# Performance work log

Measured on AMD Instinct MI355X. Metric: run time of the kernel, lower is better.

Reference implementation:

```python
import jax, jax.numpy as jnp
import numpy as np

N = 50000      # nodes
E = 800000     # edges
IN, HID, OUT = 256, 512, 256
EPS = 1e-5     # BatchNorm eps


def setup_inputs() -> dict:
    key = jax.random.key(0)
    ks = jax.random.split(key, 12)
    x = jax.random.normal(ks[0], (N, IN), jnp.float32)
    edge_index = jax.random.randint(ks[1], (2, E), 0, N, jnp.int32)

    def lin(k, fi, fo):
        return jax.random.normal(k, (fi, fo), jnp.float32) / np.sqrt(fi).astype(np.float32)

    return {
        "x": x,
        "edge_index": edge_index,
        "W1": lin(ks[2], IN, HID),  "b1": jnp.zeros((HID,), jnp.float32),
        "g1": jnp.ones((HID,), jnp.float32), "be1": jnp.zeros((HID,), jnp.float32),
        "W2": lin(ks[3], HID, HID), "b2": jnp.zeros((HID,), jnp.float32),
        "g2": jnp.ones((HID,), jnp.float32), "be2": jnp.zeros((HID,), jnp.float32),
        "W3": lin(ks[4], HID, OUT), "b3": jnp.zeros((OUT,), jnp.float32),
    }


def _gcn_conv(x, W, b, src, dst, dinv):
    # PyG GCNConv: D^{-1/2}(A+I)D^{-1/2} X W + b, edge weights = 1
    h = x @ W                                   # [N, F_out] dense transform
    norm = (dinv[src] * dinv[dst])[:, None]     # [E, 1]
    agg = jax.ops.segment_sum(h[src] * norm, dst, num_segments=N)
    agg = agg + h * (dinv * dinv)[:, None]      # self-loop contribution
    return agg + b


def _bn(h, g, b):
    # BatchNorm1d, training-mode batch statistics over node dim
    m = h.mean(axis=0)
    v = h.var(axis=0)
    return (h - m) * jax.lax.rsqrt(v + EPS) * g + b


def reference(x, edge_index, W1, b1, g1, be1, W2, b2, g2, be2, W3, b3):
    src, dst = edge_index[0], edge_index[1]
    # symmetric normalization degrees (incl. self loop)
    deg = jax.ops.segment_sum(jnp.ones((E,), jnp.float32), dst, num_segments=N) + 1.0
    dinv = jax.lax.rsqrt(deg)

    residual = x  # in_feats == out_feats -> nn.Identity
    h = jax.nn.relu(_bn(_gcn_conv(x, W1, b1, src, dst, dinv), g1, be1))
    h = jax.nn.relu(_bn(_gcn_conv(h, W2, b2, src, dst, dinv), g2, be2))
    h = _gcn_conv(h, W3, b3, src, dst, dinv)
    return h + residual
```

## Files before the change

### kernel.cpp

```cpp
#include <hip/hip_runtime.h>
#include <hip/hip_bf16.h>

#define NN 50000
#define NE 800000

typedef unsigned short u16;
typedef unsigned int   u32;

typedef __attribute__((ext_vector_type(8))) __bf16 bf16x8;
typedef __attribute__((ext_vector_type(4))) float  f32x4;

__device__ __forceinline__ float bf2f(u16 x) {
    u32 u = ((u32)x) << 16;
    return __builtin_bit_cast(float, u);
}
__device__ __forceinline__ u16 f2bf(float f) {
    u32 u = __builtin_bit_cast(u32, f);
    u32 r = (u + 0x7FFFu + ((u >> 16) & 1u)) >> 16;
    return (u16)r;
}
__device__ __forceinline__ float bflo(u32 w) { return __builtin_bit_cast(float, w << 16); }
__device__ __forceinline__ float bfhi(u32 w) { return __builtin_bit_cast(float, w & 0xffff0000u); }

__device__ __forceinline__ int rl_i(int v, int j) {
    return __builtin_amdgcn_readlane(v, j);
}
__device__ __forceinline__ float rl_f(float v, int j) {
    return __builtin_bit_cast(float, __builtin_amdgcn_readlane(__builtin_bit_cast(int, v), j));
}

__device__ __forceinline__ void glds16(const u16* g, u16* l) {
    __builtin_amdgcn_global_load_lds((const __attribute__((address_space(1))) void*)g,
                                     (__attribute__((address_space(3))) void*)l, 16, 0, 0);
}


__global__ __launch_bounds__(256) void count_k(const int* __restrict__ dst, int* __restrict__ deg, int E) {
    int e = blockIdx.x * 256 + threadIdx.x;
    if (e < E) atomicAdd(&deg[dst[e]], 1);
}

__global__ __launch_bounds__(256) void scan1_k(const int* __restrict__ deg, float* __restrict__ dinv,
                                               int* __restrict__ bsum, int n) {
    __shared__ int sd[256];
    int i = blockIdx.x * 256 + threadIdx.x;
    int v = (i < n) ? deg[i] : 0;
    if (i < n) dinv[i] = rsqrtf((float)v + 1.0f);
    sd[threadIdx.x] = v;
    __syncthreads();
    for (int s = 128; s > 0; s >>= 1) {
        if (threadIdx.x < s) sd[threadIdx.x] += sd[threadIdx.x + s];
        __syncthreads();
    }
    if (threadIdx.x == 0) bsum[blockIdx.x] = sd[0];
}

__global__ __launch_bounds__(256) void scan2_k(int* __restrict__ bsum, int nb) {
    __shared__ int sd[256];
    int t = threadIdx.x;
    int v = (t < nb) ? bsum[t] : 0;
    sd[t] = v;
    __syncthreads();
    for (int off = 1; off < 256; off <<= 1) {
        int tv = (t >= off) ? sd[t - off] : 0;
        __syncthreads();
        sd[t] += tv;
        __syncthreads();
    }
    if (t < nb) bsum[t] = sd[t] - v;
}

__global__ __launch_bounds__(256) void scan3_k(const int* __restrict__ deg, const int* __restrict__ bofs,
                                               int* __restrict__ rs, int* __restrict__ cur, int n) {
    __shared__ int sd[256];
    int t = threadIdx.x;
    int i = blockIdx.x * 256 + t;
    int v = (i < n) ? deg[i] : 0;
    sd[t] = v;
    __syncthreads();
    for (int off = 1; off < 256; off <<= 1) {
        int tv = (t >= off) ? sd[t - off] : 0;
        __syncthreads();
        sd[t] += tv;
        __syncthreads();
    }
    int excl = sd[t] - v + bofs[blockIdx.x];
    if (i < n) { rs[i] = excl; cur[i] = excl; }
}

__global__ __launch_bounds__(256) void fill_k(const int* __restrict__ src, const int* __restrict__ dst,
                                              int* __restrict__ cur, int* __restrict__ csr, int E) {
    int e = blockIdx.x * 256 + threadIdx.x;
    if (e < E) {
        int d = dst[e];
        int pos = atomicAdd(&cur[d], 1);
        csr[pos] = src[e];
    }
}


__global__ __launch_bounds__(256) void cast_k(const float* __restrict__ X, u16* __restrict__ Y, int total) {
    int idx = (blockIdx.x * 256 + threadIdx.x) * 8;
    if (idx >= total) return;
    float4 a = *(const float4*)(X + idx);
    float4 b = *(const float4*)(X + idx + 4);
    uint4 o;
    o.x = (u32)f2bf(a.x) | ((u32)f2bf(a.y) << 16);
    o.y = (u32)f2bf(a.z) | ((u32)f2bf(a.w) << 16);
    o.z = (u32)f2bf(b.x) | ((u32)f2bf(b.y) << 16);
    o.w = (u32)f2bf(b.z) | ((u32)f2bf(b.w) << 16);
    *(uint4*)(Y + idx) = o;
}


__global__ __launch_bounds__(256) void transpose_all_k(const float* __restrict__ W1, u16* __restrict__ W1t,
                                                       const float* __restrict__ W2, u16* __restrict__ W2t,
                                                       const float* __restrict__ W3, u16* __restrict__ W3t) {
    int b = blockIdx.x;
    const float* W; u16* Wt; int K, F, t;
    if (b < 128)      { W = W1; Wt = W1t; K = 256; F = 512; t = b; }
    else if (b < 384) { W = W2; Wt = W2t; K = 512; F = 512; t = b - 128; }
    else              { W = W3; Wt = W3t; K = 512; F = 256; t = b - 384; }
    const int kt = K / 32;
    const int k0 = (t % kt) * 32, f0 = (t / kt) * 32;
    __shared__ float tt[32][33];
    int tx = threadIdx.x & 31, ty = threadIdx.x >> 5;
    for (int r = ty; r < 32; r += 8) tt[r][tx] = W[(size_t)(k0 + r) * F + f0 + tx];
    __syncthreads();
    for (int r = ty; r < 32; r += 8) Wt[(size_t)(f0 + r) * K + k0 + tx] = f2bf(tt[tx][r]);
}


__global__ __launch_bounds__(256) void agg2_k(const u16* __restrict__ X, u16* __restrict__ Y,
                                              const float* __restrict__ dinv, const int* __restrict__ rs,
                                              const int* __restrict__ dg, const int* __restrict__ csr,
                                              const float* __restrict__ cs, const float* __restrict__ cq,
                                              const float* __restrict__ g, const float* __restrict__ be,
                                              int base) {
    __shared__ float lsc[512], lsh[512];
    const int tid = threadIdx.x;
    for (int f = tid; f < 512; f += 256) {
        float m = cs[f] * (1.f / NN);
        float v = cq[f] * (1.f / NN) - m * m;
        float s = rsqrtf(v + 1e-5f) * g[f];
        lsc[f] = s;
        lsh[f] = be[f] - m * s;
    }
    __syncthreads();

    const int lane = tid & 63;
    const int i = __builtin_amdgcn_readfirstlane(base + blockIdx.x * 4 + (tid >> 6));
    if (i >= NN) return;
    const int start = rs[i], cnt = dg[i];
    const float di = dinv[i];

    float sc[8], sh[8];
    #pragma unroll
    for (int k = 0; k < 8; k++) {
        sc[k] = lsc[lane * 8 + k];
        sh[k] = lsh[lane * 8 + k];
    }

    float acc[8];
    #pragma unroll
    for (int k = 0; k < 8; k++) acc[k] = 0.f;

    auto gadd = [&](int row, float wgt) {
        const u16* p = X + (size_t)row * 512 + lane * 8;
        uint4 q = *(const uint4*)p;
        float v[8];
        v[0] = bflo(q.x); v[1] = bfhi(q.x);
        v[2] = bflo(q.y); v[3] = bfhi(q.y);
        v[4] = bflo(q.z); v[5] = bfhi(q.z);
        v[6] = bflo(q.w); v[7] = bfhi(q.w);
        #pragma unroll
        for (int k = 0; k < 8; k++) {
            float x = fmaxf(fmaf(v[k], sc[k], sh[k]), 0.f);
            acc[k] = fmaf(x, wgt, acc[k]);
        }
    };

    gadd(i, di);

    for (int bse = 0; bse < cnt; bse += 64) {
        const int m = min(64, cnt - bse);
        int   sidx = 0;
        float sw   = 0.f;
        if (lane < m) {
            sidx = csr[start + bse + lane];
            sw   = dinv[sidx];
        }
        int j = 0;
        for (; j + 8 <= m; j += 8) {
            int   r[8];
            float w[8];
            #pragma unroll
            for (int q = 0; q < 8; q++) {
                r[q] = rl_i(sidx, j + q);
                w[q] = rl_f(sw, j + q);
            }
            #pragma unroll
            for (int q = 0; q < 8; q++) gadd(r[q], w[q]);
        }
        for (; j < m; j++) gadd(rl_i(sidx, j), rl_f(sw, j));
    }

    uint4 o;
    o.x = (u32)f2bf(acc[0] * di) | ((u32)f2bf(acc[1] * di) << 16);
    o.y = (u32)f2bf(acc[2] * di) | ((u32)f2bf(acc[3] * di) << 16);
    o.z = (u32)f2bf(acc[4] * di) | ((u32)f2bf(acc[5] * di) << 16);
    o.w = (u32)f2bf(acc[6] * di) | ((u32)f2bf(acc[7] * di) << 16);
    *(uint4*)(Y + (size_t)i * 512 + lane * 8) = o;
}


template <int MODE>
__global__ __launch_bounds__(256) void aggp_k(const u16* __restrict__ X, u16* __restrict__ Y,
                                              float* __restrict__ Yf,
                                              const float* __restrict__ dinv, const int* __restrict__ rs,
                                              const int* __restrict__ dg, const int* __restrict__ csr,
                                              const float* __restrict__ b3, const float* __restrict__ xres) {
    const int tid  = threadIdx.x;
    const int lane = tid & 63;
    const int hf   = lane >> 5;
    const int fl   = lane & 31;
    const int i = blockIdx.x * 4 + (tid >> 6);
    if (i >= NN) return;
    const int start = rs[i], cnt = dg[i];
    const float di = dinv[i];

    float acc[8];
    #pragma unroll
    for (int k = 0; k < 8; k++) acc[k] = 0.f;

    auto gadd = [&](int row, float wgt) {
        uint4 q = *(const uint4*)(X + (size_t)row * 256 + fl * 8);
        float v[8];
        v[0] = bflo(q.x); v[1] = bfhi(q.x);
        v[2] = bflo(q.y); v[3] = bfhi(q.y);
        v[4] = bflo(q.z); v[5] = bfhi(q.z);
        v[6] = bflo(q.w); v[7] = bfhi(q.w);
        #pragma unroll
        for (int k = 0; k < 8; k++) acc[k] = fmaf(v[k], wgt, acc[k]);
    };

    gadd(i, hf ? 0.f : di);

    for (int bse = 0; bse < cnt; bse += 64) {
        const int m = min(64, cnt - bse);
        int   sidx = 0;
        float sw   = 0.f;
        if (lane < m) {
            sidx = csr[start + bse + lane];
            sw   = dinv[sidx];
        }
        int j = 0;
        for (; j + 8 <= m; j += 8) {
            int   r0 = __shfl(sidx, j + 0 + hf), r1 = __shfl(sidx, j + 2 + hf);
            int   r2 = __shfl(sidx, j + 4 + hf), r3 = __shfl(sidx, j + 6 + hf);
            float w0 = __shfl(sw, j + 0 + hf), w1 = __shfl(sw, j + 2 + hf);
            float w2 = __shfl(sw, j + 4 + hf), w3 = __shfl(sw, j + 6 + hf);
            gadd(r0, w0);
            gadd(r1, w1);
            gadd(r2, w2);
            gadd(r3, w3);
        }
        for (; j < m; j += 2) {
            gadd(__shfl(sidx, j + hf), __shfl(sw, j + hf));
        }
    }

    #pragma unroll
    for (int k = 0; k < 8; k++) acc[k] += __shfl_xor(acc[k], 32);

    if (hf == 0) {
        if constexpr (MODE == 2) {
            const float* xr = xres + (size_t)i * 256 + fl * 8;
            float4 x0 = *(const float4*)xr;
            float4 x1 = *(const float4*)(xr + 4);
            float4 b0 = *(const float4*)(b3 + fl * 8);
            float4 b1 = *(const float4*)(b3 + fl * 8 + 4);
            float4 o0, o1;
            o0.x = acc[0] * di + b0.x + x0.x; o0.y = acc[1] * di + b0.y + x0.y;
            o0.z = acc[2] * di + b0.z + x0.z; o0.w = acc[3] * di + b0.w + x0.w;
            o1.x = acc[4] * di + b1.x + x1.x; o1.y = acc[5] * di + b1.y + x1.y;
            o1.z = acc[6] * di + b1.z + x1.z; o1.w = acc[7] * di + b1.w + x1.w;
            float* yp = Yf + (size_t)i * 256 + fl * 8;
            *(float4*)yp = o0;
            *(float4*)(yp + 4) = o1;
        } else {
            uint4 o;
            o.x = (u32)f2bf(acc[0] * di) | ((u32)f2bf(acc[1] * di) << 16);
            o.y = (u32)f2bf(acc[2] * di) | ((u32)f2bf(acc[3] * di) << 16);
            o.z = (u32)f2bf(acc[4] * di) | ((u32)f2bf(acc[5] * di) << 16);
            o.w = (u32)f2bf(acc[6] * di) | ((u32)f2bf(acc[7] * di) << 16);
            *(uint4*)(Y + (size_t)i * 256 + fl * 8) = o;
        }
    }
}


template <bool STATS, bool BIAS>
__global__ __launch_bounds__(256) void gemm_k(const u16* __restrict__ A, const u16* __restrict__ Wt,
                                              const float* __restrict__ bias, u16* __restrict__ C,
                                              float* __restrict__ colsum, float* __restrict__ colsq,
                                              int M, int K, int F) {
    __shared__ u16 As[128 * 32];
    __shared__ u16 Bs[128 * 32];
    const int m0 = blockIdx.x * 128, f0 = blockIdx.y * 128;
    const int tid = threadIdx.x;
    const int lane = tid & 63, wave = tid >> 6;
    const int waveM = (wave >> 1) * 64, waveN = (wave & 1) * 64;
    const int lrow = tid >> 2;
    const int lch  = (tid & 3) ^ ((tid >> 3) & 3);

    f32x4 acc[4][4];
    const f32x4 fz = {0.f, 0.f, 0.f, 0.f};
    #pragma unroll
    for (int i = 0; i < 4; i++)
        #pragma unroll
        for (int j = 0; j < 4; j++) acc[i][j] = fz;

    const int rA0 = m0 + lrow, rA1 = m0 + 64 + lrow;
    const int cA0 = (rA0 < M) ? rA0 : (M - 1);
    const int cA1 = (rA1 < M) ? rA1 : (M - 1);
    const u16* pA0 = A + (size_t)cA0 * K + lch * 8;
    const u16* pA1 = A + (size_t)cA1 * K + lch * 8;
    const u16* pB0 = Wt + (size_t)(f0 + lrow) * K + lch * 8;
    const u16* pB1 = Wt + (size_t)(f0 + 64 + lrow) * K + lch * 8;
    u16* qA0 = &As[tid * 8];
    u16* qA1 = &As[2048 + tid * 8];
    u16* qB0 = &Bs[tid * 8];
    u16* qB1 = &Bs[2048 + tid * 8];

    const int fm = lane & 15, fq = lane >> 4;
    const int fqs = fq ^ ((fm >> 1) & 3);

    for (int k0 = 0; k0 < K; k0 += 32) {
        __syncthreads();
        glds16(pA0 + k0, qA0);
        glds16(pA1 + k0, qA1);
        glds16(pB0 + k0, qB0);
        glds16(pB1 + k0, qB1);
        __syncthreads();
        bf16x8 af[4], bfr[4];
        #pragma unroll
        for (int i = 0; i < 4; i++)
            af[i] = *(const bf16x8*)&As[(waveM + i * 16 + fm) * 32 + fqs * 8];
        #pragma unroll
        for (int j = 0; j < 4; j++)
            bfr[j] = *(const bf16x8*)&Bs[(waveN + j * 16 + fm) * 32 + fqs * 8];
        #pragma unroll
        for (int i = 0; i < 4; i++)
            #pragma unroll
            for (int j = 0; j < 4; j++)
                acc[i][j] = __builtin_amdgcn_mfma_f32_16x16x32_bf16(af[i], bfr[j], acc[i][j], 0, 0, 0);
    }

    #pragma unroll
    for (int j = 0; j < 4; j++) {
        const int col = f0 + waveN + j * 16 + fm;
        const float bcol = BIAS ? bias[col] : 0.f;
        float s = 0.f, s2 = 0.f;
        #pragma unroll
        for (int i = 0; i < 4; i++) {
            const int rb = m0 + waveM + i * 16 + fq * 4;
            #pragma unroll
            for (int r = 0; r < 4; r++) {
                const int row = rb + r;
                if (row < M) {
                    float v = acc[i][j][r] + bcol;
                    C[(size_t)row * F + col] = f2bf(v);
                    if (STATS) { s += v; s2 += v * v; }
                }
            }
        }
        if (STATS) {
            s += __shfl_xor(s, 16);
            s += __shfl_xor(s, 32);
            s2 += __shfl_xor(s2, 16);
            s2 += __shfl_xor(s2, 32);
            if (fq == 0) {
                atomicAdd(&colsum[col], s);
                atomicAdd(&colsq[col], s2);
            }
        }
    }
}


__global__ __launch_bounds__(256) void bnrelu_k(u16* __restrict__ H,
                                                const float* __restrict__ cs, const float* __restrict__ cq,
                                                const float* __restrict__ g, const float* __restrict__ be,
                                                int total) {
    __shared__ float lsc[512], lsh[512];
    const int t = threadIdx.x;
    for (int f = t; f < 512; f += 256) {
        float m = cs[f] * (1.f / NN);
        float v = cq[f] * (1.f / NN) - m * m;
        float s = rsqrtf(v + 1e-5f) * g[f];
        lsc[f] = s;
        lsh[f] = be[f] - m * s;
    }
    __syncthreads();

    int idx = blockIdx.x * 256 + t;
    int base = idx * 8;
    if (base >= total) return;
    uint4 p = *(const uint4*)(H + base);
    int col = base & 511;
    u32 w[4] = {p.x, p.y, p.z, p.w};
    u32 o[4];
    #pragma unroll
    for (int q = 0; q < 4; q++) {
        float x0 = fmaxf(fmaf(bflo(w[q]), lsc[col + 2 * q], lsh[col + 2 * q]), 0.f);
        float x1 = fmaxf(fmaf(bfhi(w[q]), lsc[col + 2 * q + 1], lsh[col + 2 * q + 1]), 0.f);
        o[q] = ((u32)f2bf(x1) << 16) | (u32)f2bf(x0);
    }
    uint4 po = {o[0], o[1], o[2], o[3]};
    *(uint4*)(H + base) = po;
}


extern "C" void kernel_launch(void* const* d_in, const int* in_sizes, int n_in,
                              void* d_out, int out_size, void* d_ws, size_t ws_size,
                              hipStream_t stream) {
    const float* x   = (const float*)d_in[0];
    const int*   ei  = (const int*)d_in[1];
    const float* W1  = (const float*)d_in[2];
    const float* b1  = (const float*)d_in[3];
    const float* pg1 = (const float*)d_in[4];
    const float* pbe1= (const float*)d_in[5];
    const float* W2  = (const float*)d_in[6];
    const float* b2  = (const float*)d_in[7];
    const float* pg2 = (const float*)d_in[8];
    const float* pbe2= (const float*)d_in[9];
    const float* W3  = (const float*)d_in[10];
    const float* b3  = (const float*)d_in[11];
    float* out = (float*)d_out;

    char* ws = (char*)d_ws;
    size_t off = 0;
    auto alloc = [&](size_t bytes) -> char* {
        char* p = ws + off;
        off += (bytes + 255) & ~(size_t)255;
        return p;
    };
    float* dinv  = (float*)alloc(NN * 4);
    int*   deg   = (int*)alloc(NN * 4);
    float* stats = (float*)alloc(4 * 512 * 4);
    float* cs1 = stats, *cq1 = stats + 512, *cs2 = stats + 1024, *cq2 = stats + 1536;
    int*   rs    = (int*)alloc(NN * 4);
    int*   cur   = (int*)alloc(NN * 4);
    int*   bsum  = (int*)alloc(256 * 4);
    int*   csr   = (int*)alloc(NE * 4);
    u16*   W1t   = (u16*)alloc((size_t)512 * 256 * 2);
    u16*   W2t   = (u16*)alloc((size_t)512 * 512 * 2);
    u16*   W3t   = (u16*)alloc((size_t)256 * 512 * 2);
    u16*   HB    = (u16*)alloc((size_t)NN * 512 * 2);
    u16*   G3    = (u16*)alloc((size_t)NN * 256 * 2);

    u16* XB = G3;
    u16* A1 = (u16*)d_out;
    u16* A2 = (u16*)d_out;

    const int* srcp = ei;
    const int* dstp = ei + NE;

    const size_t degAligned = ((size_t)NN * 4 + 255) & ~(size_t)255;
    hipMemsetAsync(deg, 0, degAligned + 4 * 512 * 4, stream);

    const int nbN = (NN + 255) / 256;
    count_k<<<(NE + 255) / 256, 256, 0, stream>>>(dstp, deg, NE);
    scan1_k<<<nbN, 256, 0, stream>>>(deg, dinv, bsum, NN);
    scan2_k<<<1, 256, 0, stream>>>(bsum, nbN);
    scan3_k<<<nbN, 256, 0, stream>>>(deg, bsum, rs, cur, NN);
    fill_k<<<(NE + 255) / 256, 256, 0, stream>>>(srcp, dstp, cur, csr, NE);

    transpose_all_k<<<512, 256, 0, stream>>>(W1, W1t, W2, W2t, W3, W3t);

    cast_k<<<NN * 256 / 8 / 256, 256, 0, stream>>>(x, XB, NN * 256);

    const int MT = (NN + 127) / 128;
    const int AGB = (NN + 3) / 4;

    aggp_k<0><<<AGB, 256, 0, stream>>>(XB, A1, nullptr, dinv, rs, deg, csr,
                                       nullptr, nullptr);
    gemm_k<true, true><<<dim3(MT, 4), 256, 0, stream>>>(A1, W1t, b1, HB, cs1, cq1, NN, 256, 512);

    agg2_k<<<AGB / 2, 256, 0, stream>>>(HB, A2, dinv, rs, deg, csr, cs1, cq1, pg1, pbe1, 0);
    agg2_k<<<AGB / 2, 256, 0, stream>>>(HB, A2, dinv, rs, deg, csr, cs1, cq1, pg1, pbe1, NN / 2);
    gemm_k<true, true><<<dim3(MT, 4), 256, 0, stream>>>(A2, W2t, b2, HB, cs2, cq2, NN, 512, 512);
    bnrelu_k<<<NN * 512 / 8 / 256, 256, 0, stream>>>(HB, cs2, cq2, pg2, pbe2, NN * 512);

    gemm_k<false, false><<<dim3(MT, 2), 256, 0, stream>>>(HB, W3t, nullptr, G3, nullptr, nullptr, NN, 512, 256);
    aggp_k<2><<<AGB, 256, 0, stream>>>(G3, nullptr, out, dinv, rs, deg, csr,
                                       b3, x);
}
```

Measured before the change: 681.6 us.

## Triple-buffer GEMM LDS staging and swap grid order for A-tile reuse

The GEMM kernel now uses three LDS buffers with async global-to-LDS loads issued two K-tiles ahead, waiting on partial vmcnt counts instead of a full sync each iteration. This lets the memory latency of the next tiles overlap the MFMA work. The grid is also transposed so blocks sharing the same A row-tile (different output column tiles) are launched adjacently, which should improve L2 reuse of A. LDS use triples to 48KB per block, which may reduce occupancy, and correctness depends on the hand-counted vmcnt values.

```diff
diff --git a/kernel.cpp b/kernel.cpp
--- a/kernel.cpp
+++ b/kernel.cpp
@@ -305,9 +305,9 @@
                                               const float* __restrict__ bias, u16* __restrict__ C,
                                               float* __restrict__ colsum, float* __restrict__ colsq,
                                               int M, int K, int F) {
-    __shared__ u16 As[128 * 32];
-    __shared__ u16 Bs[128 * 32];
-    const int m0 = blockIdx.x * 128, f0 = blockIdx.y * 128;
+    __shared__ u16 As[3][128 * 32];
+    __shared__ u16 Bs[3][128 * 32];
+    const int f0 = blockIdx.x * 128, m0 = blockIdx.y * 128;
     const int tid = threadIdx.x;
     const int lane = tid & 63, wave = tid >> 6;
     const int waveM = (wave >> 1) * 64, waveN = (wave & 1) * 64;
@@ -328,33 +328,46 @@
     const u16* pA1 = A + (size_t)cA1 * K + lch * 8;
     const u16* pB0 = Wt + (size_t)(f0 + lrow) * K + lch * 8;
     const u16* pB1 = Wt + (size_t)(f0 + 64 + lrow) * K + lch * 8;
-    u16* qA0 = &As[tid * 8];
-    u16* qA1 = &As[2048 + tid * 8];
-    u16* qB0 = &Bs[tid * 8];
-    u16* qB1 = &Bs[2048 + tid * 8];
+
+    auto stage = [&](int tile, int buf) {
+        const int k0 = tile * 32;
+        glds16(pA0 + k0, &As[buf][tid * 8]);
+        glds16(pA1 + k0, &As[buf][2048 + tid * 8]);
+        glds16(pB0 + k0, &Bs[buf][tid * 8]);
+        glds16(pB1 + k0, &Bs[buf][2048 + tid * 8]);
+    };
 
     const int fm = lane & 15, fq = lane >> 4;
     const int fqs = fq ^ ((fm >> 1) & 3);
 
-    for (int k0 = 0; k0 < K; k0 += 32) {
-        __syncthreads();
-        glds16(pA0 + k0, qA0);
-        glds16(pA1 + k0, qA1);
-        glds16(pB0 + k0, qB0);
-        glds16(pB1 + k0, qB1);
-        __syncthreads();
+    const int nt = K / 32;
+    stage(0, 0);
+    stage(1, 1);
+    int b0 = 0, b1 = 1, b2 = 2;
+
+    for (int t = 0; t < nt; ++t) {
+        if (t + 2 < nt) stage(t + 2, b2);
+        const int rem = nt - 1 - t;
+        if (rem >= 2)      asm volatile("s_waitcnt vmcnt(8)" ::: "memory");
+        else if (rem == 1) asm volatile("s_waitcnt vmcnt(4)" ::: "memory");
+        else               asm volatile("s_waitcnt vmcnt(0)" ::: "memory");
+        __builtin_amdgcn_s_barrier();
+        asm volatile("" ::: "memory");
         bf16x8 af[4], bfr[4];
         #pragma unroll
         for (int i = 0; i < 4; i++)
-            af[i] = *(const bf16x8*)&As[(waveM + i * 16 + fm) * 32 + fqs * 8];
+            af[i] = *(const bf16x8*)&As[b0][(waveM + i * 16 + fm) * 32 + fqs * 8];
         #pragma unroll
         for (int j = 0; j < 4; j++)
-            bfr[j] = *(const bf16x8*)&Bs[(waveN + j * 16 + fm) * 32 + fqs * 8];
+            bfr[j] = *(const bf16x8*)&Bs[b0][(waveN + j * 16 + fm) * 32 + fqs * 8];
         #pragma unroll
         for (int i = 0; i < 4; i++)
             #pragma unroll
             for (int j = 0; j < 4; j++)
                 acc[i][j] = __builtin_amdgcn_mfma_f32_16x16x32_bf16(af[i], bfr[j], acc[i][j], 0, 0, 0);
+        asm volatile("" ::: "memory");
+        __builtin_amdgcn_s_barrier();
+        const int tmp = b0; b0 = b1; b1 = b2; b2 = tmp;
     }
 
     #pragma unroll
@@ -486,14 +499,14 @@
 
     aggp_k<0><<<AGB, 256, 0, stream>>>(XB, A1, nullptr, dinv, rs, deg, csr,
                                        nullptr, nullptr);
-    gemm_k<true, true><<<dim3(MT, 4), 256, 0, stream>>>(A1, W1t, b1, HB, cs1, cq1, NN, 256, 512);
+    gemm_k<true, true><<<dim3(4, MT), 256, 0, stream>>>(A1, W1t, b1, HB, cs1, cq1, NN, 256, 512);
 
     agg2_k<<<AGB / 2, 256, 0, stream>>>(HB, A2, dinv, rs, deg, csr, cs1, cq1, pg1, pbe1, 0);
     agg2_k<<<AGB / 2, 256, 0, stream>>>(HB, A2, dinv, rs, deg, csr, cs1, cq1, pg1, pbe1, NN / 2);
-    gemm_k<true, true><<<dim3(MT, 4), 256, 0, stream>>>(A2, W2t, b2, HB, cs2, cq2, NN, 512, 512);
+    gemm_k<true, true><<<dim3(4, MT), 256, 0, stream>>>(A2, W2t, b2, HB, cs2, cq2, NN, 512, 512);
     bnrelu_k<<<NN * 512 / 8 / 256, 256, 0, stream>>>(HB, cs2, cq2, pg2, pbe2, NN * 512);
 
-    gemm_k<false, false><<<dim3(MT, 2), 256, 0, stream>>>(HB, W3t, nullptr, G3, nullptr, nullptr, NN, 512, 256);
+    gemm_k<false, false><<<dim3(2, MT), 256, 0, stream>>>(HB, W3t, nullptr, G3, nullptr, nullptr, NN, 512, 256);
     aggp_k<2><<<AGB, 256, 0, stream>>>(G3, nullptr, out, dinv, rs, deg, csr,
                                        b3, x);
 }
```

After: 654.8 us. 3.9% less time.
